# Performance work log

Hardware: AMD Instinct MI355X
Metric: run time of the kernel (lower is better)

The kernel has to match this reference:

```python
import jax, jax.numpy as jnp
import numpy as np

B, T = 2, 2048
D_MODEL, D_HIDDEN = 1024, 2048
N_EXPERTS, TOP_K = 8, 2
N_TOKENS = B * T
CAPACITY = 2 * N_TOKENS * TOP_K // N_EXPERTS  # 4096


def setup_inputs() -> dict:
    key = jax.random.key(0)
    k_x, k_rw, k_w, k_v, k_o = jax.random.split(key, 5)
    x = jax.random.normal(k_x, (B, T, D_MODEL), jnp.float32)
    # router: nn.Linear(d_model, n_experts) -> weight [E, D], bias [E]
    router_w = jax.random.normal(k_rw, (N_EXPERTS, D_MODEL), jnp.float32) * D_MODEL ** -0.5
    router_b = jnp.zeros((N_EXPERTS,), jnp.float32)
    # stacked expert params, matching SwiGLU init scales
    W = jax.random.normal(k_w, (N_EXPERTS, D_MODEL, D_HIDDEN), jnp.float32) * D_MODEL ** -0.5
    V = jax.random.normal(k_v, (N_EXPERTS, D_MODEL, D_HIDDEN), jnp.float32) * D_MODEL ** -0.5
    W_out = jax.random.normal(k_o, (N_EXPERTS, D_HIDDEN, D_MODEL), jnp.float32) * D_HIDDEN ** -0.5
    return {"x": x, "router_w": router_w, "router_b": router_b, "W": W, "V": V, "W_out": W_out}


def reference(x, router_w, router_b, W, V, W_out):
    Bq, Tq, D = x.shape
    N = Bq * Tq
    x_flat = x.reshape(N, D)

    # token-level top-k routing
    router_logits = x_flat @ router_w.T + router_b            # [N, E]
    top_vals, top_ids = jax.lax.top_k(router_logits, TOP_K)   # [N, K]
    top_probs = jax.nn.softmax(top_vals, axis=-1)             # [N, K]

    # pad row N: gathers with fill index N read zeros / contribute zero weight
    x_pad = jnp.concatenate([x_flat, jnp.zeros((1, D), x_flat.dtype)], axis=0)
    probs_pad = jnp.concatenate([top_probs, jnp.zeros((1, TOP_K), top_probs.dtype)], axis=0)

    out = jnp.zeros((N + 1, D), x_flat.dtype)
    for e in range(N_EXPERTS):  # static small loop over experts
        tok, slot = jnp.nonzero(top_ids == e, size=CAPACITY, fill_value=(N, 0))
        w = probs_pad[tok, slot][:, None]     # [C, 1], zero for padding slots
        xin = x_pad[tok]                      # [C, D] gather
        a = xin @ W[e]                        # [C, H]
        b = xin @ V[e]                        # [C, H]
        y = (a * (b * jax.nn.sigmoid(b))) @ W_out[e]  # SwiGLU: a * swish(b) -> [C, D]
        out = out.at[tok].add(y * w)          # weighted scatter-add
    return out[:N].reshape(Bq, Tq, D)
```

## Files before the change

### kernel.cpp

```cpp
#include <hip/hip_runtime.h>
#include <cstdint>
#include <cstddef>

#define N_TOK 4096
#define DM    1024
#define DH    2048
#define NE    8
#define NSLOT 8192

typedef short bf16x8_t __attribute__((ext_vector_type(8)));
typedef float f32x4    __attribute__((ext_vector_type(4)));

__device__ __forceinline__ unsigned short f2bf(float f) {
  union { float f; unsigned int u; } v; v.f = f;
  unsigned int u = v.u;
  u += 0x7fffu + ((u >> 16) & 1u);
  return (unsigned short)(u >> 16);
}

#define GLD16(gp, lp)                                                          \
  __builtin_amdgcn_global_load_lds(                                            \
      (const __attribute__((address_space(1))) void*)(gp),                     \
      (__attribute__((address_space(3))) void*)(lp), 16, 0, 0)

__global__ __launch_bounds__(256) void k_transpose_bf16(
    const float* __restrict__ src, unsigned short* __restrict__ dst,
    int R, int C, long srcEStride, long dstEStride, int dstRowOff) {
  const int e = blockIdx.z;
  const float* s = src + (size_t)e * srcEStride;
  unsigned short* d = dst + (size_t)e * dstEStride;
  const int c0 = blockIdx.x * 32, r0 = blockIdx.y * 32;
  __shared__ float tile[32][33];
  const int tx = threadIdx.x & 31, ty = threadIdx.x >> 5;
#pragma unroll
  for (int j = 0; j < 4; j++) {
    const int r = ty + j * 8;
    tile[r][tx] = s[(size_t)(r0 + r) * C + c0 + tx];
  }
  __syncthreads();
#pragma unroll
  for (int j = 0; j < 4; j++) {
    const int r = ty + j * 8;
    d[(size_t)(dstRowOff + c0 + r) * R + r0 + tx] = f2bf(tile[tx][r]);
  }
}

__global__ __launch_bounds__(256) void k_router(
    const float* __restrict__ x, const float* __restrict__ rw,
    const float* __restrict__ rb, int* __restrict__ counts,
    int* __restrict__ meta_e, int* __restrict__ meta_idx,
    float* __restrict__ meta_p) {
  const int wv = threadIdx.x >> 6;
  const int l  = threadIdx.x & 63;
  const int tk = blockIdx.x * 4 + wv;
  const float* xr = x + (size_t)tk * DM;

  float acc[NE];
#pragma unroll
  for (int e = 0; e < NE; e++) acc[e] = 0.f;
#pragma unroll 4
  for (int i = 0; i < DM / 64; i++) {
    const float xv = xr[i * 64 + l];
#pragma unroll
    for (int e = 0; e < NE; e++) acc[e] += xv * rw[e * DM + i * 64 + l];
  }
#pragma unroll
  for (int off = 32; off > 0; off >>= 1) {
#pragma unroll
    for (int e = 0; e < NE; e++) acc[e] += __shfl_xor(acc[e], off);
  }
#pragma unroll
  for (int e = 0; e < NE; e++) acc[e] += rb[e];

  float v0 = -1e30f; int e0 = 0;
#pragma unroll
  for (int e = 0; e < NE; e++) { if (acc[e] > v0) { v0 = acc[e]; e0 = e; } }
  float v1 = -1e30f; int e1 = 0;
#pragma unroll
  for (int e = 0; e < NE; e++) { if (e != e0 && acc[e] > v1) { v1 = acc[e]; e1 = e; } }
  const float p0 = 1.0f / (1.0f + __expf(v1 - v0));
  const float p1 = 1.0f - p0;

  if (l == 0) {
    const int i0 = atomicAdd(&counts[e0], 1);
    const int i1 = atomicAdd(&counts[e1], 1);
    meta_e[tk * 2 + 0] = e0;  meta_e[tk * 2 + 1] = e1;
    meta_idx[tk * 2 + 0] = i0; meta_idx[tk * 2 + 1] = i1;
    meta_p[tk * 2 + 0] = p0;  meta_p[tk * 2 + 1] = p1;
  }
}

__global__ void k_prefix(const int* __restrict__ counts, int* __restrict__ offsets) {
  if (threadIdx.x == 0) {
    int s = 0;
#pragma unroll
    for (int e = 0; e < NE; e++) { offsets[e] = s; s += counts[e]; }
  }
}

__global__ __launch_bounds__(256) void k_gather(
    const float* __restrict__ x, const int* __restrict__ meta_e,
    const int* __restrict__ meta_idx, const float* __restrict__ meta_p,
    const int* __restrict__ offsets, unsigned short* __restrict__ Xg,
    int* __restrict__ tok_of_slot, float* __restrict__ wt_of_slot) {
  const int s = blockIdx.x;
  const int tk = s >> 1;
  const int e = meta_e[s];
  const int gslot = offsets[e] + meta_idx[s];
  if (threadIdx.x == 0) {
    tok_of_slot[gslot] = tk;
    wt_of_slot[gslot] = meta_p[s];
  }
  const float4 v = ((const float4*)(x + (size_t)tk * DM))[threadIdx.x];
  ushort4 o;
  o.x = f2bf(v.x); o.y = f2bf(v.y); o.z = f2bf(v.z); o.w = f2bf(v.w);
  *(ushort4*)(Xg + (size_t)gslot * DM + threadIdx.x * 4) = o;
}

__global__ __launch_bounds__(256, 2) void k_gemm1(
    const unsigned short* __restrict__ Xg, const unsigned short* __restrict__ B1t,
    unsigned short* __restrict__ G, const int* __restrict__ counts,
    const int* __restrict__ offsets) {
  const int e = blockIdx.z;
  const int mt = blockIdx.y;
  const int cnt = counts[e];
  if (mt * 128 >= cnt) return;
  const int h0 = blockIdx.x * 128;
  const int off = offsets[e];
  const int row_base = off + mt * 128;

  __shared__ unsigned short As[128 * 32];
  __shared__ unsigned short Ws[128 * 32];
  __shared__ unsigned short Vs[128 * 32];

  const int t = threadIdx.x;
  const int l = t & 63;
  const int w = t >> 6;
  const int wm = (w >> 1) * 64;
  const int wn = (w & 1) * 64;
  const int lr = l & 15;
  const int kq = (l >> 4) * 8;

  const unsigned short* Bw = B1t + ((size_t)e * 4096 + h0) * DM;
  const unsigned short* Bv = Bw + (size_t)DH * DM;

  const int c0 = t, c1 = t + 256;
  const int ar0 = c0 >> 2, ak0 = (c0 & 3) * 8;
  const int ar1 = c1 >> 2, ak1 = (c1 & 3) * 8;
  const int arow0 = min(row_base + ar0, NSLOT - 1);
  const int arow1 = min(row_base + ar1, NSLOT - 1);

  f32x4 acc_a[4][4], acc_b[4][4];
  const f32x4 z4 = {0.f, 0.f, 0.f, 0.f};
#pragma unroll
  for (int i = 0; i < 4; i++)
#pragma unroll
    for (int j = 0; j < 4; j++) { acc_a[i][j] = z4; acc_b[i][j] = z4; }

  for (int k0 = 0; k0 < DM; k0 += 32) {
    __syncthreads();
    GLD16(Xg + (size_t)arow0 * DM + k0 + ak0, As + c0 * 8);
    GLD16(Xg + (size_t)arow1 * DM + k0 + ak1, As + c1 * 8);
    GLD16(Bw + (size_t)ar0 * DM + k0 + ak0, Ws + c0 * 8);
    GLD16(Bw + (size_t)ar1 * DM + k0 + ak1, Ws + c1 * 8);
    GLD16(Bv + (size_t)ar0 * DM + k0 + ak0, Vs + c0 * 8);
    GLD16(Bv + (size_t)ar1 * DM + k0 + ak1, Vs + c1 * 8);
    __syncthreads();

    bf16x8_t af[4], wf[4], vf[4];
#pragma unroll
    for (int mi = 0; mi < 4; mi++)
      af[mi] = *(const bf16x8_t*)&As[(wm + mi * 16 + lr) * 32 + kq];
#pragma unroll
    for (int ni = 0; ni < 4; ni++) {
      wf[ni] = *(const bf16x8_t*)&Ws[(wn + ni * 16 + lr) * 32 + kq];
      vf[ni] = *(const bf16x8_t*)&Vs[(wn + ni * 16 + lr) * 32 + kq];
    }
#pragma unroll
    for (int mi = 0; mi < 4; mi++)
#pragma unroll
      for (int ni = 0; ni < 4; ni++) {
        acc_a[mi][ni] = __builtin_amdgcn_mfma_f32_16x16x32_bf16(af[mi], wf[ni], acc_a[mi][ni], 0, 0, 0);
        acc_b[mi][ni] = __builtin_amdgcn_mfma_f32_16x16x32_bf16(af[mi], vf[ni], acc_b[mi][ni], 0, 0, 0);
      }
  }

  const int q4 = (l >> 4) * 4;
#pragma unroll
  for (int mi = 0; mi < 4; mi++) {
#pragma unroll
    for (int r = 0; r < 4; r++) {
      const int mloc = mt * 128 + wm + mi * 16 + q4 + r;
      if (mloc >= cnt) continue;
      unsigned short* grow = G + (size_t)(off + mloc) * DH;
#pragma unroll
      for (int ni = 0; ni < 4; ni++) {
        const int h = h0 + wn + ni * 16 + lr;
        const float a = acc_a[mi][ni][r];
        const float b = acc_b[mi][ni][r];
        const float s = b / (1.0f + __expf(-b));
        grow[h] = f2bf(a * s);
      }
    }
  }
}

__global__ __launch_bounds__(256, 2) void k_gemm2(
    const unsigned short* __restrict__ G, const unsigned short* __restrict__ B2t,
    float* __restrict__ out, const int* __restrict__ counts,
    const int* __restrict__ offsets, const int* __restrict__ tok_of_slot,
    const float* __restrict__ wt_of_slot) {
  const int e = blockIdx.z;
  const int mt = blockIdx.y;
  const int cnt = counts[e];
  if (mt * 128 >= cnt) return;
  const int n0 = blockIdx.x * 128;
  const int off = offsets[e];
  const int row_base = off + mt * 128;

  __shared__ unsigned short As[128 * 32];
  __shared__ unsigned short Bs[128 * 32];

  const int t = threadIdx.x;
  const int l = t & 63;
  const int w = t >> 6;
  const int wm = (w >> 1) * 64;
  const int wn = (w & 1) * 64;
  const int lr = l & 15;
  const int kq = (l >> 4) * 8;

  const unsigned short* Bp = B2t + ((size_t)e * DM + n0) * DH;

  const int c0 = t, c1 = t + 256;
  const int ar0 = c0 >> 2, ak0 = (c0 & 3) * 8;
  const int ar1 = c1 >> 2, ak1 = (c1 & 3) * 8;
  const int arow0 = min(row_base + ar0, NSLOT - 1);
  const int arow1 = min(row_base + ar1, NSLOT - 1);

  f32x4 acc[4][4];
  const f32x4 z4 = {0.f, 0.f, 0.f, 0.f};
#pragma unroll
  for (int i = 0; i < 4; i++)
#pragma unroll
    for (int j = 0; j < 4; j++) acc[i][j] = z4;

  for (int k0 = 0; k0 < DH; k0 += 32) {
    __syncthreads();
    GLD16(G + (size_t)arow0 * DH + k0 + ak0, As + c0 * 8);
    GLD16(G + (size_t)arow1 * DH + k0 + ak1, As + c1 * 8);
    GLD16(Bp + (size_t)ar0 * DH + k0 + ak0, Bs + c0 * 8);
    GLD16(Bp + (size_t)ar1 * DH + k0 + ak1, Bs + c1 * 8);
    __syncthreads();

    bf16x8_t af[4], bf[4];
#pragma unroll
    for (int mi = 0; mi < 4; mi++)
      af[mi] = *(const bf16x8_t*)&As[(wm + mi * 16 + lr) * 32 + kq];
#pragma unroll
    for (int ni = 0; ni < 4; ni++)
      bf[ni] = *(const bf16x8_t*)&Bs[(wn + ni * 16 + lr) * 32 + kq];
#pragma unroll
    for (int mi = 0; mi < 4; mi++)
#pragma unroll
      for (int ni = 0; ni < 4; ni++)
        acc[mi][ni] = __builtin_amdgcn_mfma_f32_16x16x32_bf16(af[mi], bf[ni], acc[mi][ni], 0, 0, 0);
  }

  const int q4 = (l >> 4) * 4;
#pragma unroll
  for (int mi = 0; mi < 4; mi++) {
#pragma unroll
    for (int r = 0; r < 4; r++) {
      const int mloc = mt * 128 + wm + mi * 16 + q4 + r;
      if (mloc >= cnt) continue;
      const int gs = off + mloc;
      const int tok = tok_of_slot[gs];
      const float wt = wt_of_slot[gs];
      float* orow = out + (size_t)tok * DM;
#pragma unroll
      for (int ni = 0; ni < 4; ni++) {
        const int n = n0 + wn + ni * 16 + lr;
        atomicAdd(&orow[n], acc[mi][ni][r] * wt);
      }
    }
  }
}

extern "C" void kernel_launch(void* const* d_in, const int* in_sizes, int n_in,
                              void* d_out, int out_size, void* d_ws, size_t ws_size,
                              hipStream_t stream) {
  const float* x    = (const float*)d_in[0];
  const float* rw   = (const float*)d_in[1];
  const float* rb   = (const float*)d_in[2];
  const float* W    = (const float*)d_in[3];
  const float* V    = (const float*)d_in[4];
  const float* Wout = (const float*)d_in[5];
  float* out = (float*)d_out;

  char* p = (char*)d_ws;
  unsigned short* B1t = (unsigned short*)p; p += (size_t)NE * 4096 * DM * 2;
  unsigned short* B2t = (unsigned short*)p; p += (size_t)NE * DM * DH * 2;
  unsigned short* Xg  = (unsigned short*)p; p += (size_t)NSLOT * DM * 2;
  unsigned short* G   = (unsigned short*)p; p += (size_t)NSLOT * DH * 2;
  int*   counts      = (int*)p;   p += 256;
  int*   offsets     = (int*)p;   p += 256;
  int*   meta_e      = (int*)p;   p += (size_t)N_TOK * 2 * 4;
  int*   meta_idx    = (int*)p;   p += (size_t)N_TOK * 2 * 4;
  float* meta_p      = (float*)p; p += (size_t)N_TOK * 2 * 4;
  int*   tok_of_slot = (int*)p;   p += (size_t)NSLOT * 4;
  float* wt_of_slot  = (float*)p; p += (size_t)NSLOT * 4;

  hipMemsetAsync(counts, 0, 256, stream);
  hipMemsetAsync(out, 0, (size_t)out_size * sizeof(float), stream);

  k_transpose_bf16<<<dim3(DH / 32, DM / 32, NE), 256, 0, stream>>>(
      W, B1t, DM, DH, (long)DM * DH, (long)4096 * DM, 0);
  k_transpose_bf16<<<dim3(DH / 32, DM / 32, NE), 256, 0, stream>>>(
      V, B1t, DM, DH, (long)DM * DH, (long)4096 * DM, DH);
  k_transpose_bf16<<<dim3(DM / 32, DH / 32, NE), 256, 0, stream>>>(
      Wout, B2t, DH, DM, (long)DH * DM, (long)DM * DH, 0);

  k_router<<<N_TOK / 4, 256, 0, stream>>>(x, rw, rb, counts, meta_e, meta_idx, meta_p);
  k_prefix<<<1, 64, 0, stream>>>(counts, offsets);
  k_gather<<<NSLOT, 256, 0, stream>>>(x, meta_e, meta_idx, meta_p, offsets, Xg,
                                      tok_of_slot, wt_of_slot);

  k_gemm1<<<dim3(DH / 128, NSLOT / 128, NE), 256, 0, stream>>>(Xg, B1t, G, counts, offsets);
  k_gemm2<<<dim3(DM / 128, NSLOT / 128, NE), 256, 0, stream>>>(G, B2t, out, counts, offsets,
                                                               tok_of_slot, wt_of_slot);
}
```

Baseline: 546.5 us.

## Replace atomic scatter-add with per-slot output and combine kernel; vectorize weight transpose

The second GEMM now writes unweighted expert outputs to a per-slot fp32 buffer that reuses the W/V bf16 workspace. A new combine kernel reads each token's two slots, weights them and writes the output directly. This removes the float atomics and the output memset. The weight transpose uses 64x64 tiles with float4 loads and 16-byte bf16 stores, and W and V are merged into one launch. The cost is an extra read and write of the 8192x1024 fp32 intermediate.

```diff
diff --git a/kernel.cpp b/kernel.cpp
--- a/kernel.cpp
+++ b/kernel.cpp
@@ -10,6 +10,7 @@
 
 typedef short bf16x8_t __attribute__((ext_vector_type(8)));
 typedef float f32x4    __attribute__((ext_vector_type(4)));
+typedef unsigned short u16x8 __attribute__((ext_vector_type(8)));
 
 __device__ __forceinline__ unsigned short f2bf(float f) {
   union { float f; unsigned int u; } v; v.f = f;
@@ -24,24 +25,38 @@
       (__attribute__((address_space(3))) void*)(lp), 16, 0, 0)
 
 __global__ __launch_bounds__(256) void k_transpose_bf16(
-    const float* __restrict__ src, unsigned short* __restrict__ dst,
-    int R, int C, long srcEStride, long dstEStride, int dstRowOff) {
-  const int e = blockIdx.z;
-  const float* s = src + (size_t)e * srcEStride;
-  unsigned short* d = dst + (size_t)e * dstEStride;
-  const int c0 = blockIdx.x * 32, r0 = blockIdx.y * 32;
-  __shared__ float tile[32][33];
-  const int tx = threadIdx.x & 31, ty = threadIdx.x >> 5;
-#pragma unroll
-  for (int j = 0; j < 4; j++) {
-    const int r = ty + j * 8;
-    tile[r][tx] = s[(size_t)(r0 + r) * C + c0 + tx];
+    const float* __restrict__ src0, const float* __restrict__ src1,
+    unsigned short* __restrict__ dst, int R, int C,
+    long srcEStride, long dstEStride, int rowOff1) {
+  const int z = blockIdx.z;
+  const int e = z & 7;
+  const bool second = z >= 8;
+  const float* s = (second ? src1 : src0) + (size_t)e * srcEStride;
+  unsigned short* d = dst + (size_t)e * dstEStride + (size_t)(second ? rowOff1 : 0) * R;
+  const int c0 = blockIdx.x * 64, r0 = blockIdx.y * 64;
+  __shared__ float tile[64][65];
+  const int t = threadIdx.x;
+  {
+    const int cc = (t & 15) * 4;
+#pragma unroll
+    for (int j = 0; j < 4; j++) {
+      const int r = (t >> 4) + j * 16;
+      const float4 v = *(const float4*)(s + (size_t)(r0 + r) * C + c0 + cc);
+      tile[r][cc + 0] = v.x; tile[r][cc + 1] = v.y;
+      tile[r][cc + 2] = v.z; tile[r][cc + 3] = v.w;
+    }
   }
   __syncthreads();
-#pragma unroll
-  for (int j = 0; j < 4; j++) {
-    const int r = ty + j * 8;
-    d[(size_t)(dstRowOff + c0 + r) * R + r0 + tx] = f2bf(tile[tx][r]);
+  {
+    const int r8 = (t & 7) * 8;
+#pragma unroll
+    for (int j = 0; j < 2; j++) {
+      const int c = (t >> 3) + j * 32;
+      u16x8 o;
+#pragma unroll
+      for (int i = 0; i < 8; i++) o[i] = f2bf(tile[r8 + i][c]);
+      *(u16x8*)(d + (size_t)(c0 + c) * R + r0 + r8) = o;
+    }
   }
 }
 
@@ -100,17 +115,12 @@
 
 __global__ __launch_bounds__(256) void k_gather(
     const float* __restrict__ x, const int* __restrict__ meta_e,
-    const int* __restrict__ meta_idx, const float* __restrict__ meta_p,
-    const int* __restrict__ offsets, unsigned short* __restrict__ Xg,
-    int* __restrict__ tok_of_slot, float* __restrict__ wt_of_slot) {
+    const int* __restrict__ meta_idx, const int* __restrict__ offsets,
+    unsigned short* __restrict__ Xg) {
   const int s = blockIdx.x;
   const int tk = s >> 1;
   const int e = meta_e[s];
   const int gslot = offsets[e] + meta_idx[s];
-  if (threadIdx.x == 0) {
-    tok_of_slot[gslot] = tk;
-    wt_of_slot[gslot] = meta_p[s];
-  }
   const float4 v = ((const float4*)(x + (size_t)tk * DM))[threadIdx.x];
   ushort4 o;
   o.x = f2bf(v.x); o.y = f2bf(v.y); o.z = f2bf(v.z); o.w = f2bf(v.w);
@@ -207,9 +217,8 @@
 
 __global__ __launch_bounds__(256, 2) void k_gemm2(
     const unsigned short* __restrict__ G, const unsigned short* __restrict__ B2t,
-    float* __restrict__ out, const int* __restrict__ counts,
-    const int* __restrict__ offsets, const int* __restrict__ tok_of_slot,
-    const float* __restrict__ wt_of_slot) {
+    float* __restrict__ Y, const int* __restrict__ counts,
+    const int* __restrict__ offsets) {
   const int e = blockIdx.z;
   const int mt = blockIdx.y;
   const int cnt = counts[e];
@@ -273,17 +282,31 @@
     for (int r = 0; r < 4; r++) {
       const int mloc = mt * 128 + wm + mi * 16 + q4 + r;
       if (mloc >= cnt) continue;
-      const int gs = off + mloc;
-      const int tok = tok_of_slot[gs];
-      const float wt = wt_of_slot[gs];
-      float* orow = out + (size_t)tok * DM;
-#pragma unroll
-      for (int ni = 0; ni < 4; ni++) {
-        const int n = n0 + wn + ni * 16 + lr;
-        atomicAdd(&orow[n], acc[mi][ni][r] * wt);
-      }
-    }
-  }
+      float* yrow = Y + (size_t)(off + mloc) * DM;
+#pragma unroll
+      for (int ni = 0; ni < 4; ni++)
+        yrow[n0 + wn + ni * 16 + lr] = acc[mi][ni][r];
+    }
+  }
+}
+
+__global__ __launch_bounds__(256) void k_combine(
+    const float* __restrict__ Y, const int* __restrict__ meta_e,
+    const int* __restrict__ meta_idx, const float* __restrict__ meta_p,
+    const int* __restrict__ offsets, float* __restrict__ out) {
+  const int tk = blockIdx.x;
+  const int s0 = tk * 2, s1 = s0 + 1;
+  const int g0 = offsets[meta_e[s0]] + meta_idx[s0];
+  const int g1 = offsets[meta_e[s1]] + meta_idx[s1];
+  const float w0 = meta_p[s0], w1 = meta_p[s1];
+  const float4 a = ((const float4*)(Y + (size_t)g0 * DM))[threadIdx.x];
+  const float4 b = ((const float4*)(Y + (size_t)g1 * DM))[threadIdx.x];
+  float4 o;
+  o.x = w0 * a.x + w1 * b.x;
+  o.y = w0 * a.y + w1 * b.y;
+  o.z = w0 * a.z + w1 * b.z;
+  o.w = w0 * a.w + w1 * b.w;
+  ((float4*)(out + (size_t)tk * DM))[threadIdx.x] = o;
 }
 
 extern "C" void kernel_launch(void* const* d_in, const int* in_sizes, int n_in,
@@ -299,6 +322,7 @@
 
   char* p = (char*)d_ws;
   unsigned short* B1t = (unsigned short*)p; p += (size_t)NE * 4096 * DM * 2;
+  float*          Y   = (float*)B1t;
   unsigned short* B2t = (unsigned short*)p; p += (size_t)NE * DM * DH * 2;
   unsigned short* Xg  = (unsigned short*)p; p += (size_t)NSLOT * DM * 2;
   unsigned short* G   = (unsigned short*)p; p += (size_t)NSLOT * DH * 2;
@@ -307,25 +331,19 @@
   int*   meta_e      = (int*)p;   p += (size_t)N_TOK * 2 * 4;
   int*   meta_idx    = (int*)p;   p += (size_t)N_TOK * 2 * 4;
   float* meta_p      = (float*)p; p += (size_t)N_TOK * 2 * 4;
-  int*   tok_of_slot = (int*)p;   p += (size_t)NSLOT * 4;
-  float* wt_of_slot  = (float*)p; p += (size_t)NSLOT * 4;
 
   hipMemsetAsync(counts, 0, 256, stream);
-  hipMemsetAsync(out, 0, (size_t)out_size * sizeof(float), stream);
-
-  k_transpose_bf16<<<dim3(DH / 32, DM / 32, NE), 256, 0, stream>>>(
-      W, B1t, DM, DH, (long)DM * DH, (long)4096 * DM, 0);
-  k_transpose_bf16<<<dim3(DH / 32, DM / 32, NE), 256, 0, stream>>>(
-      V, B1t, DM, DH, (long)DM * DH, (long)4096 * DM, DH);
-  k_transpose_bf16<<<dim3(DM / 32, DH / 32, NE), 256, 0, stream>>>(
-      Wout, B2t, DH, DM, (long)DH * DM, (long)DM * DH, 0);
+
+  k_transpose_bf16<<<dim3(DH / 64, DM / 64, 2 * NE), 256, 0, stream>>>(
+      W, V, B1t, DM, DH, (long)DM * DH, (long)4096 * DM, DH);
+  k_transpose_bf16<<<dim3(DM / 64, DH / 64, NE), 256, 0, stream>>>(
+      Wout, Wout, B2t, DH, DM, (long)DH * DM, (long)DM * DH, 0);
 
   k_router<<<N_TOK / 4, 256, 0, stream>>>(x, rw, rb, counts, meta_e, meta_idx, meta_p);
   k_prefix<<<1, 64, 0, stream>>>(counts, offsets);
-  k_gather<<<NSLOT, 256, 0, stream>>>(x, meta_e, meta_idx, meta_p, offsets, Xg,
-                                      tok_of_slot, wt_of_slot);
+  k_gather<<<NSLOT, 256, 0, stream>>>(x, meta_e, meta_idx, offsets, Xg);
 
   k_gemm1<<<dim3(DH / 128, NSLOT / 128, NE), 256, 0, stream>>>(Xg, B1t, G, counts, offsets);
-  k_gemm2<<<dim3(DM / 128, NSLOT / 128, NE), 256, 0, stream>>>(G, B2t, out, counts, offsets,
-                                                               tok_of_slot, wt_of_slot);
-}
+  k_gemm2<<<dim3(DM / 128, NSLOT / 128, NE), 256, 0, stream>>>(G, B2t, Y, counts, offsets);
+  k_combine<<<N_TOK, 256, 0, stream>>>(Y, meta_e, meta_idx, meta_p, offsets, out);
+}
```

New measurement: 532.9 us. 2.5% less time.
